# Kernel tuning notes

Measured on AMD Instinct MI355X. Metric: run time of the kernel, lower is better.

The kernel has to match this reference:

```python
import math
import jax, jax.numpy as jnp
import numpy as np

B = 8          # number of graphs in the batch
NMAX = 256     # max nodes per graph (padding size)
K = 128        # num_kernels
H = 32         # num_heads
NTYPE = 101    # max_node_type + 1


def setup_inputs() -> dict:
    key = jax.random.key(0)
    ks = jax.random.split(key, 10)
    sizes = np.asarray(NMAX - np.arange(B) * 16, dtype=np.int32)  # 256,240,...,144 -> ragged
    N = int(sizes.sum())  # 1600
    coord = jax.random.normal(ks[0], (N, 3), dtype=jnp.float32) * 3.0
    node_type = jax.random.randint(ks[1], (N,), 0, NTYPE, dtype=jnp.int32)
    gaussian_means = jax.random.uniform(ks[2], (1, K), minval=0.0, maxval=3.0, dtype=jnp.float32)
    gaussian_stds = jax.random.uniform(ks[3], (1, K), minval=0.0, maxval=3.0, dtype=jnp.float32)
    # nn.Embedding(max_node_type+1, 2) tables; original init is const(0)/const(1),
    # we perturb so the computation is non-degenerate.
    mul_w = jax.random.normal(ks[4], (NTYPE, 2), dtype=jnp.float32) * 0.1
    bias_w = 1.0 + jax.random.normal(ks[5], (NTYPE, 2), dtype=jnp.float32) * 0.1
    W1 = jax.random.normal(ks[6], (K, K), dtype=jnp.float32) / math.sqrt(K)
    b1 = jnp.zeros((K,), dtype=jnp.float32)
    W2 = jax.random.normal(ks[7], (K, H), dtype=jnp.float32) / math.sqrt(K)
    b2 = jnp.zeros((H,), dtype=jnp.float32)
    return {
        "coord": coord,
        "gaussian_means": gaussian_means,
        "gaussian_stds": gaussian_stds,
        "mul_w": mul_w,
        "bias_w": bias_w,
        "W1": W1,
        "b1": b1,
        "W2": W2,
        "b2": b2,
        "node_type": node_type,
        "batch_num_nodes": jnp.asarray(sizes),
    }


def reference(coord, gaussian_means, gaussian_stds, mul_w, bias_w, W1, b1, W2, b2,
              node_type, batch_num_nodes):
    N = coord.shape[0]
    offsets = jnp.concatenate([jnp.zeros((1,), dtype=batch_num_nodes.dtype),
                               jnp.cumsum(batch_num_nodes)[:-1]])
    ar = jnp.arange(NMAX)
    idx = offsets[:, None] + ar[None, :]                     # [B, n] flat node index per graph slot
    valid = ar[None, :] < batch_num_nodes[:, None]           # [B, n] node mask
    idx_c = jnp.clip(idx, 0, N - 1)
    pc = coord[idx_c]                                        # [B, n, 3] padded coords
    pt = node_type[idx_c]                                    # [B, n]

    # pairwise Euclidean distance (torch.cdist p=2), sqrt-safe at 0
    diff = pc[:, :, None, :] - pc[:, None, :, :]             # [B, n, n, 3]
    sq = jnp.sum(diff * diff, axis=-1)                       # [B, n, n]
    nz = sq > 0
    dist = jnp.where(nz, jnp.sqrt(jnp.where(nz, sq, 1.0)), 0.0)

    # outer-sum of per-node (src, dst) scaling embeddings
    mul_e = mul_w[pt]                                        # [B, n, 2]
    bias_e = bias_w[pt]
    mul = mul_e[:, :, None, 0] + mul_e[:, None, :, 1]        # [B, n, n]
    bias = bias_e[:, :, None, 0] + bias_e[:, None, :, 1]
    scaled = mul * dist + bias                               # [B, n, n]

    means = gaussian_means.reshape(-1)                       # [K]
    stds = jnp.abs(gaussian_stds.reshape(-1)) + 0.01         # [K]
    z = (scaled[..., None] - means) / stds                   # [B, n, n, K]
    gk = jnp.exp(-0.5 * z * z) / (-math.sqrt(2.0 * math.pi) * stds)

    h = jax.nn.gelu(gk @ W1 + b1, approximate=False)         # exact gelu like torch F.gelu
    out = h @ W2 + b2                                        # [B, n, n, H]

    pair = valid[:, :, None] & valid[:, None, :]             # padded positions -> -inf
    return jnp.where(pair[..., None], out, -jnp.inf)
```

## Files before the change

kernel.cpp:

```cpp
#include <hip/hip_runtime.h>
#include <math.h>

#define NMAXC 256
#define KC 128
#define HC 32
#define BC 8
#define TP 128
#define NEG_SENTINEL (-1.0e30f)

typedef __bf16 bf16x8 __attribute__((ext_vector_type(8)));
typedef float  f32x16 __attribute__((ext_vector_type(16)));

union FragU { uint4 u; bf16x8 v; };

__device__ __forceinline__ unsigned pack_bf16(float f0, float f1) {
    return (__float_as_uint(f0) >> 16) | (__float_as_uint(f1) & 0xFFFF0000u);
}

__global__ __launch_bounds__(256) void se3d_prep(const float* __restrict__ W1,
                                                 const float* __restrict__ W2,
                                                 uint4* __restrict__ wsv) {
    int t = blockIdx.x * 256 + threadIdx.x;
    if (t < 2048) {
        int fb = t >> 6, lane = t & 63;
        int nt = fb >> 3, ks = fb & 7;
        int n  = nt * 32 + (lane & 31);
        int k0 = ks * 16 + 8 * (lane >> 5);
        unsigned u[4];
#pragma unroll
        for (int p = 0; p < 4; ++p)
            u[p] = pack_bf16(W1[(k0 + 2 * p) * KC + n], W1[(k0 + 2 * p + 1) * KC + n]);
        wsv[t] = make_uint4(u[0], u[1], u[2], u[3]);
    } else if (t < 2560) {
        int c = t - 2048;
        int ks = c >> 6, lane = c & 63;
        int n  = lane & 31;
        int k0 = ks * 16 + 8 * (lane >> 5);
        unsigned u[4];
#pragma unroll
        for (int p = 0; p < 4; ++p)
            u[p] = pack_bf16(W2[(k0 + 2 * p) * HC + n], W2[(k0 + 2 * p + 1) * HC + n]);
        wsv[2048 + c] = make_uint4(u[0], u[1], u[2], u[3]);
    }
}

__global__ __launch_bounds__(256) void se3d_fill_invalid(float* __restrict__ out,
                                                         const int* __restrict__ bnn) {
    int idx = blockIdx.x * 256 + threadIdx.x;
    int b = idx >> 16;
    int rem = idx & 65535;
    int i = rem >> 8, j = rem & 255;
    int n = bnn[b];
    if (i >= n || j >= n) {
        float4 v = make_float4(NEG_SENTINEL, NEG_SENTINEL, NEG_SENTINEL, NEG_SENTINEL);
        float4* o = (float4*)(out + (size_t)idx * HC);
#pragma unroll
        for (int t = 0; t < HC / 4; ++t) o[t] = v;
    }
}

__global__ __launch_bounds__(256, 4) void se3d_main(
    const float* __restrict__ coord, const float* __restrict__ gm,
    const float* __restrict__ gs, const float* __restrict__ mulw,
    const float* __restrict__ biasw, const float* __restrict__ b1,
    const float* __restrict__ b2, const int* __restrict__ ntype,
    const int* __restrict__ bnn, const void* __restrict__ ws,
    float* __restrict__ out)
{
    __shared__ __attribute__((aligned(16))) unsigned short hS[4 * 32 * 136];
    __shared__ float scaled[TP];
    __shared__ int   obase[TP];
    __shared__ float kmeanS[KC], kinvS[KC], knegS[KC];

    const int b = blockIdx.y;
    const int n = bnn[b];
    const int q0 = blockIdx.x * TP;
    if (q0 >= n * n) return;

    int off = 0;
    for (int t = 0; t < b; ++t) off += bnn[t];
    const int tid = threadIdx.x;

    if (tid < KC) {
        float std = fabsf(gs[tid]) + 0.01f;
        float inv = __builtin_amdgcn_rcpf(std);
        kmeanS[tid] = gm[tid];
        kinvS[tid]  = inv;
        knegS[tid]  = -0.3989422804014327f * inv;
        int q = q0 + tid;
        int i = q / n;
        int j = q - i * n;
        int gi = off + i, gj = off + j;
        float dx = coord[gi * 3 + 0] - coord[gj * 3 + 0];
        float dy = coord[gi * 3 + 1] - coord[gj * 3 + 1];
        float dz = coord[gi * 3 + 2] - coord[gj * 3 + 2];
        float sq = dx * dx + dy * dy + dz * dz;
        float dist = sq > 0.f ? sqrtf(sq) : 0.f;
        int ti = ntype[gi], tj = ntype[gj];
        scaled[tid] = (mulw[ti * 2 + 0] + mulw[tj * 2 + 1]) * dist
                    + (biasw[ti * 2 + 0] + biasw[tj * 2 + 1]);
        obase[tid]  = ((b * NMAXC + i) * NMAXC + j) * HC;
    }
    __syncthreads();

    const int l = tid & 63, w = tid >> 6;
    const int hi = l >> 5, ln31 = l & 31;
    const int m0 = w * 32;
    const float sA = scaled[m0 + ln31];

    const bf16x8* wsW1 = (const bf16x8*)ws;
    const bf16x8* wsW2 = (const bf16x8*)((const char*)ws + 32768);

    f32x16 acc[4];
#pragma unroll
    for (int nt = 0; nt < 4; ++nt)
#pragma unroll
        for (int r = 0; r < 16; ++r) acc[nt][r] = 0.f;

    const float4* km4 = (const float4*)kmeanS;
    const float4* ki4 = (const float4*)kinvS;
    const float4* kn4 = (const float4*)knegS;

#pragma unroll
    for (int ks = 0; ks < 8; ++ks) {
        int b4 = ks * 4 + 2 * hi;
        float4 mA = km4[b4], mB = km4[b4 + 1];
        float4 iA = ki4[b4], iB = ki4[b4 + 1];
        float4 nA = kn4[b4], nB = kn4[b4 + 1];
        float g[8];
        {
            float z;
            z = (sA - mA.x) * iA.x; g[0] = __expf(-0.5f * z * z) * nA.x;
            z = (sA - mA.y) * iA.y; g[1] = __expf(-0.5f * z * z) * nA.y;
            z = (sA - mA.z) * iA.z; g[2] = __expf(-0.5f * z * z) * nA.z;
            z = (sA - mA.w) * iA.w; g[3] = __expf(-0.5f * z * z) * nA.w;
            z = (sA - mB.x) * iB.x; g[4] = __expf(-0.5f * z * z) * nB.x;
            z = (sA - mB.y) * iB.y; g[5] = __expf(-0.5f * z * z) * nB.y;
            z = (sA - mB.z) * iB.z; g[6] = __expf(-0.5f * z * z) * nB.z;
            z = (sA - mB.w) * iB.w; g[7] = __expf(-0.5f * z * z) * nB.w;
        }
        FragU a;
        a.u.x = pack_bf16(g[0], g[1]);
        a.u.y = pack_bf16(g[2], g[3]);
        a.u.z = pack_bf16(g[4], g[5]);
        a.u.w = pack_bf16(g[6], g[7]);
#pragma unroll
        for (int nt = 0; nt < 4; ++nt) {
            bf16x8 bb = wsW1[(nt * 8 + ks) * 64 + l];
            acc[nt] = __builtin_amdgcn_mfma_f32_32x32x16_bf16(a.v, bb, acc[nt], 0, 0, 0);
        }
    }

    unsigned short* hW = hS + w * (32 * 136);
#pragma unroll
    for (int nt = 0; nt < 4; ++nt) {
        float b1v = b1[nt * 32 + ln31];
#pragma unroll
        for (int r = 0; r < 16; ++r) {
            float x = acc[nt][r] + b1v;
            float targ = 0.7978845608028654f * (x + 0.044715f * x * x * x);
            float e = __expf(2.0f * targ);
            float th = 1.0f - 2.0f * __builtin_amdgcn_rcpf(e + 1.0f);
            float gl = 0.5f * x * (1.0f + th);
            int rw = (r & 3) + 8 * (r >> 2) + 4 * hi;
            hW[rw * 136 + nt * 32 + ln31] = (unsigned short)(__float_as_uint(gl) >> 16);
        }
    }

    f32x16 c2;
#pragma unroll
    for (int r = 0; r < 16; ++r) c2[r] = 0.f;
#pragma unroll
    for (int ks = 0; ks < 8; ++ks) {
        bf16x8 av = *(const bf16x8*)(hW + ln31 * 136 + ks * 16 + 8 * hi);
        bf16x8 bv = wsW2[ks * 64 + l];
        c2 = __builtin_amdgcn_mfma_f32_32x32x16_bf16(av, bv, c2, 0, 0, 0);
    }

    float b2v = b2[ln31];
#pragma unroll
    for (int r = 0; r < 16; ++r) {
        int m = m0 + (r & 3) + 8 * (r >> 2) + 4 * hi;
        out[(size_t)obase[m] + ln31] = c2[r] + b2v;
    }
}

extern "C" void kernel_launch(void* const* d_in, const int* in_sizes, int n_in,
                              void* d_out, int out_size, void* d_ws, size_t ws_size,
                              hipStream_t stream) {
    const float* coord = (const float*)d_in[0];
    const float* gm    = (const float*)d_in[1];
    const float* gs    = (const float*)d_in[2];
    const float* mulw  = (const float*)d_in[3];
    const float* biasw = (const float*)d_in[4];
    const float* W1    = (const float*)d_in[5];
    const float* b1    = (const float*)d_in[6];
    const float* W2    = (const float*)d_in[7];
    const float* b2    = (const float*)d_in[8];
    const int* ntype   = (const int*)d_in[9];
    const int* bnn     = (const int*)d_in[10];
    float* out = (float*)d_out;

    hipLaunchKernelGGL(se3d_prep, dim3(10), dim3(256), 0, stream,
                       W1, W2, (uint4*)d_ws);
    hipLaunchKernelGGL(se3d_fill_invalid, dim3(BC * NMAXC * NMAXC / 256), dim3(256),
                       0, stream, out, bnn);
    hipLaunchKernelGGL(se3d_main, dim3(NMAXC * NMAXC / TP, BC), dim3(256),
                       0, stream,
                       coord, gm, gs, mulw, biasw, b1, b2, ntype, bnn, d_ws, out);
}
```

Before: 140.7 us.

## Fuse padding fill into main kernel and simplify Gaussian and GELU math

Drops the separate invalid-fill kernel. Thread blocks whose tile falls past n*n now write the -1e30 sentinel for padded pairs, remapped through an index over the invalid region. The Gaussian basis is rewritten as exp2 of a quadratic in the scaled distance, with per-kernel coefficients precomputed once in the prep kernel. The tanh GELU is replaced by the sigmoid approximation x*sigmoid(1.702x), and both biases are folded into the accumulator initialisation. The remapping only covers every padded position when n*n is a multiple of 128, and the sigmoid GELU adds approximation error compared with exact erf GELU.

```diff
diff --git a/kernel.cpp b/kernel.cpp
--- a/kernel.cpp
+++ b/kernel.cpp
@@ -7,19 +7,27 @@
 #define BC 8
 #define TP 128
 #define NEG_SENTINEL (-1.0e30f)
+#define LOG2E 1.4426950408889634f
 
 typedef __bf16 bf16x8 __attribute__((ext_vector_type(8)));
 typedef float  f32x16 __attribute__((ext_vector_type(16)));
-
 union FragU { uint4 u; bf16x8 v; };
 
-__device__ __forceinline__ unsigned pack_bf16(float f0, float f1) {
-    return (__float_as_uint(f0) >> 16) | (__float_as_uint(f1) & 0xFFFF0000u);
+#if __has_builtin(__builtin_amdgcn_exp2f)
+#define EXP2F(x) __builtin_amdgcn_exp2f(x)
+#else
+#define EXP2F(x) exp2f(x)
+#endif
+
+__device__ __forceinline__ unsigned pack2(float lo, float hi) {
+    return __builtin_amdgcn_perm(__float_as_uint(hi), __float_as_uint(lo), 0x07060302u);
 }
 
 __global__ __launch_bounds__(256) void se3d_prep(const float* __restrict__ W1,
                                                  const float* __restrict__ W2,
-                                                 uint4* __restrict__ wsv) {
+                                                 const float* __restrict__ gm,
+                                                 const float* __restrict__ gs,
+                                                 unsigned* __restrict__ wsu) {
     int t = blockIdx.x * 256 + threadIdx.x;
     if (t < 2048) {
         int fb = t >> 6, lane = t & 63;
@@ -29,8 +37,8 @@
         unsigned u[4];
 #pragma unroll
         for (int p = 0; p < 4; ++p)
-            u[p] = pack_bf16(W1[(k0 + 2 * p) * KC + n], W1[(k0 + 2 * p + 1) * KC + n]);
-        wsv[t] = make_uint4(u[0], u[1], u[2], u[3]);
+            u[p] = pack2(W1[(k0 + 2 * p) * KC + n], W1[(k0 + 2 * p + 1) * KC + n]);
+        ((uint4*)wsu)[t] = make_uint4(u[0], u[1], u[2], u[3]);
     } else if (t < 2560) {
         int c = t - 2048;
         int ks = c >> 6, lane = c & 63;
@@ -39,29 +47,23 @@
         unsigned u[4];
 #pragma unroll
         for (int p = 0; p < 4; ++p)
-            u[p] = pack_bf16(W2[(k0 + 2 * p) * HC + n], W2[(k0 + 2 * p + 1) * HC + n]);
-        wsv[2048 + c] = make_uint4(u[0], u[1], u[2], u[3]);
-    }
-}
-
-__global__ __launch_bounds__(256) void se3d_fill_invalid(float* __restrict__ out,
-                                                         const int* __restrict__ bnn) {
-    int idx = blockIdx.x * 256 + threadIdx.x;
-    int b = idx >> 16;
-    int rem = idx & 65535;
-    int i = rem >> 8, j = rem & 255;
-    int n = bnn[b];
-    if (i >= n || j >= n) {
-        float4 v = make_float4(NEG_SENTINEL, NEG_SENTINEL, NEG_SENTINEL, NEG_SENTINEL);
-        float4* o = (float4*)(out + (size_t)idx * HC);
-#pragma unroll
-        for (int t = 0; t < HC / 4; ++t) o[t] = v;
+            u[p] = pack2(W2[(k0 + 2 * p) * HC + n], W2[(k0 + 2 * p + 1) * HC + n]);
+        ((uint4*)wsu)[2048 + c] = make_uint4(u[0], u[1], u[2], u[3]);
+    } else if (t < 2688) {
+        int k = t - 2560;
+        float inv = 1.0f / (fabsf(gs[k]) + 0.01f);
+        float m  = gm[k];
+        float A2 = -0.5f * inv * inv * LOG2E;
+        float* wf = (float*)wsu + 10240;
+        wf[k]       = A2;
+        wf[128 + k] = -2.0f * A2 * m;
+        wf[256 + k] = A2 * m * m;
+        wf[384 + k] = -0.3989422804014327f * inv;
     }
 }
 
 __global__ __launch_bounds__(256, 4) void se3d_main(
-    const float* __restrict__ coord, const float* __restrict__ gm,
-    const float* __restrict__ gs, const float* __restrict__ mulw,
+    const float* __restrict__ coord, const float* __restrict__ mulw,
     const float* __restrict__ biasw, const float* __restrict__ b1,
     const float* __restrict__ b2, const int* __restrict__ ntype,
     const int* __restrict__ bnn, const void* __restrict__ ws,
@@ -70,23 +72,37 @@
     __shared__ __attribute__((aligned(16))) unsigned short hS[4 * 32 * 136];
     __shared__ float scaled[TP];
     __shared__ int   obase[TP];
-    __shared__ float kmeanS[KC], kinvS[KC], knegS[KC];
+    __shared__ float cA[KC], cB[KC], cC[KC], cS[KC];
 
     const int b = blockIdx.y;
     const int n = bnn[b];
     const int q0 = blockIdx.x * TP;
-    if (q0 >= n * n) return;
+    const int tid = threadIdx.x;
+
+    if (q0 >= n * n) {
+        int v = q0 + (tid >> 1) - n * n;
+        int wdt = 256 - n;
+        int na = n * wdt;
+        int i, j;
+        if (v < na) { i = v / wdt; j = n + (v - i * wdt); }
+        else        { int vp = v - na; i = n + (vp >> 8); j = vp & 255; }
+        float4 s4 = make_float4(NEG_SENTINEL, NEG_SENTINEL, NEG_SENTINEL, NEG_SENTINEL);
+        float4* o = (float4*)(out + ((size_t)((b * NMAXC + i) * NMAXC + j)) * HC)
+                  + (tid & 1) * 4;
+#pragma unroll
+        for (int t = 0; t < 4; ++t) o[t] = s4;
+        return;
+    }
 
     int off = 0;
     for (int t = 0; t < b; ++t) off += bnn[t];
-    const int tid = threadIdx.x;
-
+
+    const float* wf = (const float*)((const char*)ws + 40960);
     if (tid < KC) {
-        float std = fabsf(gs[tid]) + 0.01f;
-        float inv = __builtin_amdgcn_rcpf(std);
-        kmeanS[tid] = gm[tid];
-        kinvS[tid]  = inv;
-        knegS[tid]  = -0.3989422804014327f * inv;
+        cA[tid] = wf[tid];
+        cB[tid] = wf[128 + tid];
+        cC[tid] = wf[256 + tid];
+        cS[tid] = wf[384 + tid];
         int q = q0 + tid;
         int i = q / n;
         int j = q - i * n;
@@ -106,44 +122,44 @@
     const int l = tid & 63, w = tid >> 6;
     const int hi = l >> 5, ln31 = l & 31;
     const int m0 = w * 32;
-    const float sA = scaled[m0 + ln31];
+    const float s = scaled[m0 + ln31];
 
     const bf16x8* wsW1 = (const bf16x8*)ws;
     const bf16x8* wsW2 = (const bf16x8*)((const char*)ws + 32768);
+    const float4* A4 = (const float4*)cA;
+    const float4* B4 = (const float4*)cB;
+    const float4* C4 = (const float4*)cC;
+    const float4* S4 = (const float4*)cS;
 
     f32x16 acc[4];
 #pragma unroll
-    for (int nt = 0; nt < 4; ++nt)
-#pragma unroll
-        for (int r = 0; r < 16; ++r) acc[nt][r] = 0.f;
-
-    const float4* km4 = (const float4*)kmeanS;
-    const float4* ki4 = (const float4*)kinvS;
-    const float4* kn4 = (const float4*)knegS;
+    for (int nt = 0; nt < 4; ++nt) {
+        float b1v = b1[nt * 32 + ln31];
+#pragma unroll
+        for (int r = 0; r < 16; ++r) acc[nt][r] = b1v;
+    }
 
 #pragma unroll
     for (int ks = 0; ks < 8; ++ks) {
         int b4 = ks * 4 + 2 * hi;
-        float4 mA = km4[b4], mB = km4[b4 + 1];
-        float4 iA = ki4[b4], iB = ki4[b4 + 1];
-        float4 nA = kn4[b4], nB = kn4[b4 + 1];
+        float4 a0 = A4[b4], a1 = A4[b4 + 1];
+        float4 q0v = B4[b4], q1 = B4[b4 + 1];
+        float4 c0 = C4[b4], c1 = C4[b4 + 1];
+        float4 s0 = S4[b4], s1 = S4[b4 + 1];
         float g[8];
-        {
-            float z;
-            z = (sA - mA.x) * iA.x; g[0] = __expf(-0.5f * z * z) * nA.x;
-            z = (sA - mA.y) * iA.y; g[1] = __expf(-0.5f * z * z) * nA.y;
-            z = (sA - mA.z) * iA.z; g[2] = __expf(-0.5f * z * z) * nA.z;
-            z = (sA - mA.w) * iA.w; g[3] = __expf(-0.5f * z * z) * nA.w;
-            z = (sA - mB.x) * iB.x; g[4] = __expf(-0.5f * z * z) * nB.x;
-            z = (sA - mB.y) * iB.y; g[5] = __expf(-0.5f * z * z) * nB.y;
-            z = (sA - mB.z) * iB.z; g[6] = __expf(-0.5f * z * z) * nB.z;
-            z = (sA - mB.w) * iB.w; g[7] = __expf(-0.5f * z * z) * nB.w;
-        }
+        g[0] = s0.x * EXP2F(fmaf(fmaf(a0.x, s, q0v.x), s, c0.x));
+        g[1] = s0.y * EXP2F(fmaf(fmaf(a0.y, s, q0v.y), s, c0.y));
+        g[2] = s0.z * EXP2F(fmaf(fmaf(a0.z, s, q0v.z), s, c0.z));
+        g[3] = s0.w * EXP2F(fmaf(fmaf(a0.w, s, q0v.w), s, c0.w));
+        g[4] = s1.x * EXP2F(fmaf(fmaf(a1.x, s, q1.x), s, c1.x));
+        g[5] = s1.y * EXP2F(fmaf(fmaf(a1.y, s, q1.y), s, c1.y));
+        g[6] = s1.z * EXP2F(fmaf(fmaf(a1.z, s, q1.z), s, c1.z));
+        g[7] = s1.w * EXP2F(fmaf(fmaf(a1.w, s, q1.w), s, c1.w));
         FragU a;
-        a.u.x = pack_bf16(g[0], g[1]);
-        a.u.y = pack_bf16(g[2], g[3]);
-        a.u.z = pack_bf16(g[4], g[5]);
-        a.u.w = pack_bf16(g[6], g[7]);
+        a.u.x = pack2(g[0], g[1]);
+        a.u.y = pack2(g[2], g[3]);
+        a.u.z = pack2(g[4], g[5]);
+        a.u.w = pack2(g[6], g[7]);
 #pragma unroll
         for (int nt = 0; nt < 4; ++nt) {
             bf16x8 bb = wsW1[(nt * 8 + ks) * 64 + l];
@@ -151,25 +167,26 @@
         }
     }
 
+    const float KSG = -1.702f * LOG2E;
     unsigned short* hW = hS + w * (32 * 136);
 #pragma unroll
     for (int nt = 0; nt < 4; ++nt) {
-        float b1v = b1[nt * 32 + ln31];
 #pragma unroll
         for (int r = 0; r < 16; ++r) {
-            float x = acc[nt][r] + b1v;
-            float targ = 0.7978845608028654f * (x + 0.044715f * x * x * x);
-            float e = __expf(2.0f * targ);
-            float th = 1.0f - 2.0f * __builtin_amdgcn_rcpf(e + 1.0f);
-            float gl = 0.5f * x * (1.0f + th);
+            float x = acc[nt][r];
+            float e = EXP2F(x * KSG);
+            float gl = x * __builtin_amdgcn_rcpf(1.0f + e);
             int rw = (r & 3) + 8 * (r >> 2) + 4 * hi;
             hW[rw * 136 + nt * 32 + ln31] = (unsigned short)(__float_as_uint(gl) >> 16);
         }
     }
 
     f32x16 c2;
-#pragma unroll
-    for (int r = 0; r < 16; ++r) c2[r] = 0.f;
+    {
+        float b2v = b2[ln31];
+#pragma unroll
+        for (int r = 0; r < 16; ++r) c2[r] = b2v;
+    }
 #pragma unroll
     for (int ks = 0; ks < 8; ++ks) {
         bf16x8 av = *(const bf16x8*)(hW + ln31 * 136 + ks * 16 + 8 * hi);
@@ -177,11 +194,10 @@
         c2 = __builtin_amdgcn_mfma_f32_32x32x16_bf16(av, bv, c2, 0, 0, 0);
     }
 
-    float b2v = b2[ln31];
 #pragma unroll
     for (int r = 0; r < 16; ++r) {
         int m = m0 + (r & 3) + 8 * (r >> 2) + 4 * hi;
-        out[(size_t)obase[m] + ln31] = c2[r] + b2v;
+        out[(size_t)obase[m] + ln31] = c2[r];
     }
 }
 
@@ -201,11 +217,9 @@
     const int* bnn     = (const int*)d_in[10];
     float* out = (float*)d_out;
 
-    hipLaunchKernelGGL(se3d_prep, dim3(10), dim3(256), 0, stream,
-                       W1, W2, (uint4*)d_ws);
-    hipLaunchKernelGGL(se3d_fill_invalid, dim3(BC * NMAXC * NMAXC / 256), dim3(256),
-                       0, stream, out, bnn);
+    hipLaunchKernelGGL(se3d_prep, dim3(11), dim3(256), 0, stream,
+                       W1, W2, gm, gs, (unsigned*)d_ws);
     hipLaunchKernelGGL(se3d_main, dim3(NMAXC * NMAXC / TP, BC), dim3(256),
                        0, stream,
-                       coord, gm, gs, mulw, biasw, b1, b2, ntype, bnn, d_ws, out);
-}
+                       coord, mulw, biasw, b1, b2, ntype, bnn, d_ws, out);
+}
```

New measurement: 119.1 us. -15.4%, faster.
